# Kernel tuning notes

Measured on AMD Instinct MI355X. Metric: run time of the kernel, lower is better.

## Reference

```python
import jax, jax.numpy as jnp
import numpy as np

B, S, H, NH = 2, 2048, 1024, 16
HD = H // NH  # 64


def rope_cos_sin(seq_len, dim, base=10000.0, dtype=jnp.float32):
    inv_freq = 1.0 / (base ** (jnp.arange(0, dim, 2, dtype=jnp.float32) / dim))
    t = jnp.arange(seq_len, dtype=jnp.float32)
    freqs = jnp.outer(t, inv_freq)              # [S, dim/2]
    emb = jnp.concatenate([freqs, freqs], -1)   # [S, dim]
    # broadcast shape [1, S, 1, dim]
    return jnp.cos(emb)[None, :, None, :].astype(dtype), jnp.sin(emb)[None, :, None, :].astype(dtype)


def rotate_half(x):
    x1, x2 = x[..., : x.shape[-1] // 2], x[..., x.shape[-1] // 2:]
    return jnp.concatenate([-x2, x1], axis=-1)


def setup_inputs() -> dict:
    key = jax.random.key(0)
    ks = jax.random.split(key, 5)
    sc = 1.0 / np.sqrt(H)
    x = jax.random.normal(ks[0], (B, S, H), jnp.float32)
    Wq = jax.random.normal(ks[1], (H, H), jnp.float32) * sc
    Wk = jax.random.normal(ks[2], (H, H), jnp.float32) * sc
    Wv = jax.random.normal(ks[3], (H, H), jnp.float32) * sc
    Wo = jax.random.normal(ks[4], (H, H), jnp.float32) * sc
    z = jnp.zeros((H,), jnp.float32)
    mask = jnp.tril(jnp.ones((S, S), bool))[None, None]  # causal [1,1,S,S]
    return {"x": x, "Wq": Wq, "bq": z, "Wk": Wk, "bk": z, "Wv": Wv, "bv": z,
            "Wo": Wo, "bo": z, "mask": mask}


def reference(x, Wq, bq, Wk, bk, Wv, bv, Wo, bo, mask):
    b, s, _ = x.shape
    q = (x @ Wq.T + bq).reshape(b, s, NH, HD)
    k = (x @ Wk.T + bk).reshape(b, s, NH, HD)
    v = (x @ Wv.T + bv).reshape(b, s, NH, HD)
    cos, sin = rope_cos_sin(s, HD, dtype=x.dtype)
    q = q * cos + rotate_half(q) * sin
    k = k * cos + rotate_half(k) * sin
    # [b, h, s, s] scores, explicit as in original
    scores = jnp.einsum("bqhd,bkhd->bhqk", q, k) / jnp.sqrt(jnp.asarray(HD, x.dtype))
    scores = jnp.where(mask, scores, jnp.asarray(-jnp.inf, x.dtype))
    attn = jax.nn.softmax(scores, axis=-1)
    out = jnp.einsum("bhqk,bkhd->bqhd", attn, v).reshape(b, s, H)
    return out @ Wo.T + bo
```

## Files before the change

kernel.cpp:

```cpp
#include <hip/hip_runtime.h>

typedef __bf16 bf16;
typedef __bf16 bf16x4 __attribute__((ext_vector_type(4)));
typedef __bf16 bf16x8 __attribute__((ext_vector_type(8)));
typedef float floatx4 __attribute__((ext_vector_type(4)));

#define MFMA16(a, b, c) __builtin_amdgcn_mfma_f32_16x16x32_bf16(a, b, c, 0, 0, 0)

__device__ __forceinline__ void load_lds16(const void* g, void* l) {
    __builtin_amdgcn_global_load_lds(
        (const __attribute__((address_space(1))) unsigned int*)g,
        (__attribute__((address_space(3))) unsigned int*)l, 16, 0, 0);
}

__device__ __forceinline__ bf16x8 scale8(bf16x8 a, float s) {
    bf16x8 o;
    #pragma unroll
    for (int i = 0; i < 8; i++) o[i] = (bf16)((float)a[i] * s);
    return o;
}

__global__ __launch_bounds__(256) void cvt_all_kernel(
    const float* __restrict__ x, const float* __restrict__ wq,
    const float* __restrict__ wk, const float* __restrict__ wv,
    const float* __restrict__ wo,
    bf16* __restrict__ xb, bf16* __restrict__ wqb, bf16* __restrict__ wkb,
    bf16* __restrict__ wvb, bf16* __restrict__ wob)
{
    int bid = blockIdx.x;
    const float* src; bf16* dst; int off;
    if (bid < 4096)      { src = x;  dst = xb;  off = bid; }
    else if (bid < 5120) { src = wq; dst = wqb; off = bid - 4096; }
    else if (bid < 6144) { src = wk; dst = wkb; off = bid - 5120; }
    else if (bid < 7168) { src = wv; dst = wvb; off = bid - 6144; }
    else                 { src = wo; dst = wob; off = bid - 7168; }
    int idx = (off * 256 + threadIdx.x) * 4;
    float4 v = *(const float4*)&src[idx];
    bf16x4 o;
    o[0] = (bf16)v.x; o[1] = (bf16)v.y; o[2] = (bf16)v.z; o[3] = (bf16)v.w;
    *(bf16x4*)&dst[idx] = o;
}

__global__ __launch_bounds__(256) void cvt_kernel(const float* __restrict__ x,
                                                  bf16* __restrict__ xb) {
    int idx = (blockIdx.x * 256 + threadIdx.x) * 4;
    float4 v = *(const float4*)&x[idx];
    bf16x4 o;
    o[0] = (bf16)v.x; o[1] = (bf16)v.y; o[2] = (bf16)v.z; o[3] = (bf16)v.w;
    *(bf16x4*)&xb[idx] = o;
}


#define STAGE_TILES(Asrc, Bsrc, arow, brow)                                   \
    _Pragma("unroll")                                                         \
    for (int t = 0; t < 4; t++) {                                             \
        int R0 = w * 32 + t * 8;                                              \
        int row = R0 + (lane >> 3);                                           \
        int gc = (lane & 7) ^ (row & 7);                                      \
        load_lds16(&Asrc[(size_t)(arow + row) * 1024 + k0 + gc * 8], &As[R0][0]); \
        load_lds16(&Bsrc[(size_t)(brow + row) * 1024 + k0 + gc * 8], &Bs[R0][0]); \
    }

__global__ __launch_bounds__(256) void gemm_qkv_fast(
    const bf16* __restrict__ xb,
    const bf16* __restrict__ Wq, const bf16* __restrict__ Wk,
    const bf16* __restrict__ Wv,
    const float* __restrict__ bq, const float* __restrict__ bk,
    const float* __restrict__ bv,
    bf16* __restrict__ q_ws, bf16* __restrict__ k_ws, bf16* __restrict__ vt_ws)
{
    int m0 = blockIdx.x * 128;
    int n0 = blockIdx.y * 128;
    int sec = n0 >> 10;
    int nw0 = n0 & 1023;
    const bf16* W     = (sec == 0) ? Wq : (sec == 1) ? Wk : Wv;
    const float* bias = (sec == 0) ? bq : (sec == 1) ? bk : bv;

    __shared__ bf16 As[128][64];
    __shared__ bf16 Bs[128][64];

    int tid = threadIdx.x;
    int lane = tid & 63, w = tid >> 6;
    int l15 = lane & 15, quad = lane >> 4;
    int wm = (w >> 1) * 64, wn = (w & 1) * 64;

    floatx4 acc[4][4];
    #pragma unroll
    for (int i = 0; i < 4; i++)
        #pragma unroll
        for (int j = 0; j < 4; j++) acc[i][j] = (floatx4){0.f, 0.f, 0.f, 0.f};

    for (int k0 = 0; k0 < 1024; k0 += 64) {
        __syncthreads();
        STAGE_TILES(xb, W, m0, nw0)
        __syncthreads();
        #pragma unroll
        for (int kk = 0; kk < 2; kk++) {
            int cb = kk * 4 + quad;
            bf16x8 af[4], bfr[4];
            #pragma unroll
            for (int mt = 0; mt < 4; mt++) {
                int row = wm + mt * 16 + l15;
                af[mt] = *(const bf16x8*)&As[row][(cb ^ (row & 7)) * 8];
            }
            #pragma unroll
            for (int nt = 0; nt < 4; nt++) {
                int row = wn + nt * 16 + l15;
                bfr[nt] = *(const bf16x8*)&Bs[row][(cb ^ (row & 7)) * 8];
            }
            #pragma unroll
            for (int mt = 0; mt < 4; mt++)
                #pragma unroll
                for (int nt = 0; nt < 4; nt++)
                    acc[mt][nt] = MFMA16(af[mt], bfr[nt], acc[mt][nt]);
        }
    }

    if (sec < 2) {
        bf16* outp = (sec == 0) ? q_ws : k_ws;
        float inv[2];
        inv[0] = __expf(-(float)l15 * (9.210340371976184f / 32.0f));
        inv[1] = __expf(-(float)(16 + l15) * (9.210340371976184f / 32.0f));
        #pragma unroll
        for (int mt = 0; mt < 4; mt++) {
            #pragma unroll
            for (int r = 0; r < 4; r++) {
                int m = m0 + wm + mt * 16 + quad * 4 + r;
                int bb = m >> 11, s = m & 2047;
                #pragma unroll
                for (int nt = 0; nt < 2; nt++) {
                    int nl1 = nw0 + wn + nt * 16 + l15;
                    int nl2 = nl1 + 32;
                    float x1 = acc[mt][nt][r] + bias[nl1];
                    float x2 = acc[mt][nt + 2][r] + bias[nl2];
                    float ang = (float)s * inv[nt];
                    float sn, cs;
                    __sincosf(ang, &sn, &cs);
                    int hh = nl1 >> 6, d = nl1 & 63;
                    size_t base = ((size_t)(bb * 16 + hh) * 2048 + s) * 64;
                    outp[base + d]      = (bf16)(x1 * cs - x2 * sn);
                    outp[base + d + 32] = (bf16)(x2 * cs + x1 * sn);
                }
            }
        }
    } else {
        #pragma unroll
        for (int mt = 0; mt < 4; mt++) {
            int mbase = m0 + wm + mt * 16 + quad * 4;
            int bb = mbase >> 11, s0 = mbase & 2047;
            #pragma unroll
            for (int nt = 0; nt < 4; nt++) {
                int nl = nw0 + wn + nt * 16 + l15;
                int hh = nl >> 6, d = nl & 63;
                bf16x4 pk;
                #pragma unroll
                for (int r = 0; r < 4; r++) pk[r] = (bf16)(acc[mt][nt][r] + bias[nl]);
                *(bf16x4*)&vt_ws[((size_t)(bb * 16 + hh) * 64 + d) * 2048 + s0] = pk;
            }
        }
    }
}

__global__ __launch_bounds__(256) void gemm_out_fast(
    const bf16* __restrict__ A, const bf16* __restrict__ W,
    const float* __restrict__ bias, float* __restrict__ out)
{
    int m0 = blockIdx.x * 128;
    int n0 = blockIdx.y * 128;

    __shared__ bf16 As[128][64];
    __shared__ bf16 Bs[128][64];

    int tid = threadIdx.x;
    int lane = tid & 63, w = tid >> 6;
    int l15 = lane & 15, quad = lane >> 4;
    int wm = (w >> 1) * 64, wn = (w & 1) * 64;

    floatx4 acc[4][4];
    #pragma unroll
    for (int i = 0; i < 4; i++)
        #pragma unroll
        for (int j = 0; j < 4; j++) acc[i][j] = (floatx4){0.f, 0.f, 0.f, 0.f};

    for (int k0 = 0; k0 < 1024; k0 += 64) {
        __syncthreads();
        STAGE_TILES(A, W, m0, n0)
        __syncthreads();
        #pragma unroll
        for (int kk = 0; kk < 2; kk++) {
            int cb = kk * 4 + quad;
            bf16x8 af[4], bfr[4];
            #pragma unroll
            for (int mt = 0; mt < 4; mt++) {
                int row = wm + mt * 16 + l15;
                af[mt] = *(const bf16x8*)&As[row][(cb ^ (row & 7)) * 8];
            }
            #pragma unroll
            for (int nt = 0; nt < 4; nt++) {
                int row = wn + nt * 16 + l15;
                bfr[nt] = *(const bf16x8*)&Bs[row][(cb ^ (row & 7)) * 8];
            }
            #pragma unroll
            for (int mt = 0; mt < 4; mt++)
                #pragma unroll
                for (int nt = 0; nt < 4; nt++)
                    acc[mt][nt] = MFMA16(af[mt], bfr[nt], acc[mt][nt]);
        }
    }

    #pragma unroll
    for (int mt = 0; mt < 4; mt++) {
        #pragma unroll
        for (int r = 0; r < 4; r++) {
            int m = m0 + wm + mt * 16 + quad * 4 + r;
            #pragma unroll
            for (int nt = 0; nt < 4; nt++) {
                int nl = n0 + wn + nt * 16 + l15;
                out[(size_t)m * 1024 + nl] = acc[mt][nt][r] + bias[nl];
            }
        }
    }
}

__global__ __launch_bounds__(256) void gemm_qkv_f32w(
    const bf16* __restrict__ xb,
    const float* __restrict__ Wq, const float* __restrict__ Wk,
    const float* __restrict__ Wv,
    const float* __restrict__ bq, const float* __restrict__ bk,
    const float* __restrict__ bv,
    bf16* __restrict__ q_ws, bf16* __restrict__ k_ws, bf16* __restrict__ vt_ws)
{
    int m0 = blockIdx.x * 128;
    int n0 = blockIdx.y * 128;
    int sec = n0 >> 10;
    int nw0 = n0 & 1023;
    const float* W    = (sec == 0) ? Wq : (sec == 1) ? Wk : Wv;
    const float* bias = (sec == 0) ? bq : (sec == 1) ? bk : bv;

    __shared__ bf16 As[128][72];
    __shared__ bf16 Bs[128][72];

    int tid = threadIdx.x;
    int lane = tid & 63, w = tid >> 6;
    int l15 = lane & 15, quad = lane >> 4;
    int wm = (w >> 1) * 64, wn = (w & 1) * 64;
    int sr = tid >> 1;
    int sk = (tid & 1) * 32;

    floatx4 acc[4][4];
    #pragma unroll
    for (int i = 0; i < 4; i++)
        #pragma unroll
        for (int j = 0; j < 4; j++) acc[i][j] = (floatx4){0.f, 0.f, 0.f, 0.f};

    for (int k0 = 0; k0 < 1024; k0 += 64) {
        __syncthreads();
        const bf16* ap = &xb[(size_t)(m0 + sr) * 1024 + k0 + sk];
        bf16x8 a0 = *(const bf16x8*)(ap);
        bf16x8 a1 = *(const bf16x8*)(ap + 8);
        bf16x8 a2 = *(const bf16x8*)(ap + 16);
        bf16x8 a3 = *(const bf16x8*)(ap + 24);
        const float* wp = &W[(size_t)(nw0 + sr) * 1024 + k0 + sk];
        bf16x8 bv_[4];
        #pragma unroll
        for (int c = 0; c < 4; c++) {
            float4 f0 = *(const float4*)(wp + c * 8);
            float4 f1 = *(const float4*)(wp + c * 8 + 4);
            bf16x8 t;
            t[0] = (bf16)f0.x; t[1] = (bf16)f0.y; t[2] = (bf16)f0.z; t[3] = (bf16)f0.w;
            t[4] = (bf16)f1.x; t[5] = (bf16)f1.y; t[6] = (bf16)f1.z; t[7] = (bf16)f1.w;
            bv_[c] = t;
        }
        *(bf16x8*)&As[sr][sk + 0]  = a0;
        *(bf16x8*)&As[sr][sk + 8]  = a1;
        *(bf16x8*)&As[sr][sk + 16] = a2;
        *(bf16x8*)&As[sr][sk + 24] = a3;
        #pragma unroll
        for (int c = 0; c < 4; c++) *(bf16x8*)&Bs[sr][sk + c * 8] = bv_[c];
        __syncthreads();
        #pragma unroll
        for (int kk = 0; kk < 64; kk += 32) {
            bf16x8 af[4], bfr[4];
            #pragma unroll
            for (int mt = 0; mt < 4; mt++)
                af[mt] = *(const bf16x8*)&As[wm + mt * 16 + l15][kk + quad * 8];
            #pragma unroll
            for (int nt = 0; nt < 4; nt++)
                bfr[nt] = *(const bf16x8*)&Bs[wn + nt * 16 + l15][kk + quad * 8];
            #pragma unroll
            for (int mt = 0; mt < 4; mt++)
                #pragma unroll
                for (int nt = 0; nt < 4; nt++)
                    acc[mt][nt] = MFMA16(af[mt], bfr[nt], acc[mt][nt]);
        }
    }

    if (sec < 2) {
        bf16* outp = (sec == 0) ? q_ws : k_ws;
        float inv[2];
        inv[0] = __expf(-(float)l15 * (9.210340371976184f / 32.0f));
        inv[1] = __expf(-(float)(16 + l15) * (9.210340371976184f / 32.0f));
        #pragma unroll
        for (int mt = 0; mt < 4; mt++) {
            #pragma unroll
            for (int r = 0; r < 4; r++) {
                int m = m0 + wm + mt * 16 + quad * 4 + r;
                int bb = m >> 11, s = m & 2047;
                #pragma unroll
                for (int nt = 0; nt < 2; nt++) {
                    int nl1 = nw0 + wn + nt * 16 + l15;
                    int nl2 = nl1 + 32;
                    float x1 = acc[mt][nt][r] + bias[nl1];
                    float x2 = acc[mt][nt + 2][r] + bias[nl2];
                    float ang = (float)s * inv[nt];
                    float sn, cs;
                    __sincosf(ang, &sn, &cs);
                    int hh = nl1 >> 6, d = nl1 & 63;
                    size_t base = ((size_t)(bb * 16 + hh) * 2048 + s) * 64;
                    outp[base + d]      = (bf16)(x1 * cs - x2 * sn);
                    outp[base + d + 32] = (bf16)(x2 * cs + x1 * sn);
                }
            }
        }
    } else {
        #pragma unroll
        for (int mt = 0; mt < 4; mt++) {
            int mbase = m0 + wm + mt * 16 + quad * 4;
            int bb = mbase >> 11, s0 = mbase & 2047;
            #pragma unroll
            for (int nt = 0; nt < 4; nt++) {
                int nl = nw0 + wn + nt * 16 + l15;
                int hh = nl >> 6, d = nl & 63;
                bf16x4 pk;
                #pragma unroll
                for (int r = 0; r < 4; r++) pk[r] = (bf16)(acc[mt][nt][r] + bias[nl]);
                *(bf16x4*)&vt_ws[((size_t)(bb * 16 + hh) * 64 + d) * 2048 + s0] = pk;
            }
        }
    }
}

__global__ __launch_bounds__(256) void gemm_out_f32w(
    const bf16* __restrict__ A, const float* __restrict__ W,
    const float* __restrict__ bias, float* __restrict__ out)
{
    int m0 = blockIdx.x * 128;
    int n0 = blockIdx.y * 128;

    __shared__ bf16 As[128][72];
    __shared__ bf16 Bs[128][72];

    int tid = threadIdx.x;
    int lane = tid & 63, w = tid >> 6;
    int l15 = lane & 15, quad = lane >> 4;
    int wm = (w >> 1) * 64, wn = (w & 1) * 64;
    int sr = tid >> 1;
    int sk = (tid & 1) * 32;

    floatx4 acc[4][4];
    #pragma unroll
    for (int i = 0; i < 4; i++)
        #pragma unroll
        for (int j = 0; j < 4; j++) acc[i][j] = (floatx4){0.f, 0.f, 0.f, 0.f};

    for (int k0 = 0; k0 < 1024; k0 += 64) {
        __syncthreads();
        const bf16* ap = &A[(size_t)(m0 + sr) * 1024 + k0 + sk];
        bf16x8 a0 = *(const bf16x8*)(ap);
        bf16x8 a1 = *(const bf16x8*)(ap + 8);
        bf16x8 a2 = *(const bf16x8*)(ap + 16);
        bf16x8 a3 = *(const bf16x8*)(ap + 24);
        const float* wp = &W[(size_t)(n0 + sr) * 1024 + k0 + sk];
        bf16x8 bv_[4];
        #pragma unroll
        for (int c = 0; c < 4; c++) {
            float4 f0 = *(const float4*)(wp + c * 8);
            float4 f1 = *(const float4*)(wp + c * 8 + 4);
            bf16x8 t;
            t[0] = (bf16)f0.x; t[1] = (bf16)f0.y; t[2] = (bf16)f0.z; t[3] = (bf16)f0.w;
            t[4] = (bf16)f1.x; t[5] = (bf16)f1.y; t[6] = (bf16)f1.z; t[7] = (bf16)f1.w;
            bv_[c] = t;
        }
        *(bf16x8*)&As[sr][sk + 0]  = a0;
        *(bf16x8*)&As[sr][sk + 8]  = a1;
        *(bf16x8*)&As[sr][sk + 16] = a2;
        *(bf16x8*)&As[sr][sk + 24] = a3;
        #pragma unroll
        for (int c = 0; c < 4; c++) *(bf16x8*)&Bs[sr][sk + c * 8] = bv_[c];
        __syncthreads();
        #pragma unroll
        for (int kk = 0; kk < 64; kk += 32) {
            bf16x8 af[4], bfr[4];
            #pragma unroll
            for (int mt = 0; mt < 4; mt++)
                af[mt] = *(const bf16x8*)&As[wm + mt * 16 + l15][kk + quad * 8];
            #pragma unroll
            for (int nt = 0; nt < 4; nt++)
                bfr[nt] = *(const bf16x8*)&Bs[wn + nt * 16 + l15][kk + quad * 8];
            #pragma unroll
            for (int mt = 0; mt < 4; mt++)
                #pragma unroll
                for (int nt = 0; nt < 4; nt++)
                    acc[mt][nt] = MFMA16(af[mt], bfr[nt], acc[mt][nt]);
        }
    }

    #pragma unroll
    for (int mt = 0; mt < 4; mt++) {
        #pragma unroll
        for (int r = 0; r < 4; r++) {
            int m = m0 + wm + mt * 16 + quad * 4 + r;
            #pragma unroll
            for (int nt = 0; nt < 4; nt++) {
                int nl = n0 + wn + nt * 16 + l15;
                out[(size_t)m * 1024 + nl] = acc[mt][nt][r] + bias[nl];
            }
        }
    }
}

__global__ __launch_bounds__(256) void attn_kernel(
    const bf16* __restrict__ q_ws, const bf16* __restrict__ k_ws,
    const bf16* __restrict__ vt_ws, bf16* __restrict__ o_ws)
{
    __shared__ bf16 Ks[64][64];
    __shared__ bf16 Vt[64][64];
    __shared__ bf16 Ps[4][16][72];

    int tid = threadIdx.x;
    int w = tid >> 6, lane = tid & 63;
    int l15 = lane & 15, quad = lane >> 4;
    int h = blockIdx.y, bb = blockIdx.z;
    int x = blockIdx.x;
    int qt = ((h < 8) == (bb == 0)) ? x : 31 - x;
    int bh = bb * 16 + h;
    const bf16* qp = q_ws + (size_t)bh * 2048 * 64;
    const bf16* kp = k_ws + (size_t)bh * 2048 * 64;
    const bf16* vp = vt_ws + (size_t)bh * 64 * 2048;
    int qrow = qt * 64 + w * 16;

    const float SCL = 0.125f * 1.4426950408889634f;
    bf16x8 qf0 = scale8(*(const bf16x8*)&qp[(size_t)(qrow + l15) * 64 + quad * 8], SCL);
    bf16x8 qf1 = scale8(*(const bf16x8*)&qp[(size_t)(qrow + l15) * 64 + 32 + quad * 8], SCL);

    const float MFIX = 20.0f;
    float l_lane = 0.f;
    floatx4 acc[4];
    #pragma unroll
    for (int nt = 0; nt < 4; nt++) acc[nt] = (floatx4){0.f, 0.f, 0.f, 0.f};

    int g0 = (w * 2) * 64 + lane;
    int g1 = (w * 2 + 1) * 64 + lane;
    int r0 = g0 >> 3, c0 = (g0 & 7) ^ (r0 & 7);
    int r1 = g1 >> 3, c1 = (g1 & 7) ^ (r1 & 7);
    bf16* ksBase0 = &Ks[0][0] + (w * 2) * 512;
    bf16* ksBase1 = &Ks[0][0] + (w * 2 + 1) * 512;
    bf16* vtBase0 = &Vt[0][0] + (w * 2) * 512;
    bf16* vtBase1 = &Vt[0][0] + (w * 2 + 1) * 512;

    for (int kt = 0; kt <= qt; kt++) {
        int kt0 = kt * 64;
        __syncthreads();
        load_lds16(&kp[(size_t)(kt0 + r0) * 64 + c0 * 8], ksBase0);
        load_lds16(&kp[(size_t)(kt0 + r1) * 64 + c1 * 8], ksBase1);
        load_lds16(&vp[(size_t)r0 * 2048 + kt0 + c0 * 8], vtBase0);
        load_lds16(&vp[(size_t)r1 * 2048 + kt0 + c1 * 8], vtBase1);
        __syncthreads();

        floatx4 st[4];
        #pragma unroll
        for (int kb = 0; kb < 4; kb++) {
            int row = kb * 16 + l15;
            int rx = row & 7;
            bf16x8 a0 = *(const bf16x8*)&Ks[row][(quad ^ rx) * 8];
            bf16x8 a1 = *(const bf16x8*)&Ks[row][((quad + 4) ^ rx) * 8];
            floatx4 z = {0.f, 0.f, 0.f, 0.f};
            z = MFMA16(a0, qf0, z);
            z = MFMA16(a1, qf1, z);
            st[kb] = z;
        }
        if (kt0 + 63 > qrow) {
            int q = qrow + l15;
            #pragma unroll
            for (int kb = 0; kb < 4; kb++)
                #pragma unroll
                for (int r = 0; r < 4; r++) {
                    int key = kt0 + kb * 16 + quad * 4 + r;
                    if (key > q) st[kb][r] = -1e30f;
                }
        }

        #pragma unroll
        for (int kb = 0; kb < 4; kb++) {
            bf16x4 pk;
            #pragma unroll
            for (int r = 0; r < 4; r++) {
                float pv = exp2f(st[kb][r] - MFIX);
                l_lane += pv;
                pk[r] = (bf16)pv;
            }
            *(bf16x4*)&Ps[w][l15][kb * 16 + quad * 4] = pk;
        }

        bf16x8 pb0 = *(const bf16x8*)&Ps[w][l15][quad * 8];
        bf16x8 pb1 = *(const bf16x8*)&Ps[w][l15][32 + quad * 8];
        #pragma unroll
        for (int nt = 0; nt < 4; nt++) {
            int row = nt * 16 + l15;
            int rx = row & 7;
            bf16x8 v0 = *(const bf16x8*)&Vt[row][(quad ^ rx) * 8];
            bf16x8 v1 = *(const bf16x8*)&Vt[row][((quad + 4) ^ rx) * 8];
            acc[nt] = MFMA16(v0, pb0, acc[nt]);
            acc[nt] = MFMA16(v1, pb1, acc[nt]);
        }
    }

    l_lane += __shfl_xor(l_lane, 16, 64);
    l_lane += __shfl_xor(l_lane, 32, 64);
    float inv = 1.f / l_lane;
    int s = qrow + l15;
    #pragma unroll
    for (int nt = 0; nt < 4; nt++) {
        bf16x4 pk;
        #pragma unroll
        for (int r = 0; r < 4; r++) pk[r] = (bf16)(acc[nt][r] * inv);
        *(bf16x4*)&o_ws[((size_t)(bb * 2048 + s)) * 1024 + h * 64 + nt * 16 + quad * 4] = pk;
    }
}

extern "C" void kernel_launch(void* const* d_in, const int* in_sizes, int n_in,
                              void* d_out, int out_size, void* d_ws, size_t ws_size,
                              hipStream_t stream) {
    const float* x  = (const float*)d_in[0];
    const float* Wq = (const float*)d_in[1];
    const float* bq = (const float*)d_in[2];
    const float* Wk = (const float*)d_in[3];
    const float* bk = (const float*)d_in[4];
    const float* Wv = (const float*)d_in[5];
    const float* bv = (const float*)d_in[6];
    const float* Wo = (const float*)d_in[7];
    const float* bo = (const float*)d_in[8];
    float* out = (float*)d_out;

    const size_t NELEM = (size_t)2 * 2048 * 1024;
    const size_t WELEM = (size_t)1024 * 1024;
    bf16* xb    = (bf16*)d_ws;
    bf16* q_ws  = xb + NELEM;
    bf16* k_ws  = q_ws + NELEM;
    bf16* vt_ws = k_ws + NELEM;
    bf16* o_ws  = xb;
    bf16* wqb   = vt_ws + NELEM;
    bf16* wkb   = wqb + WELEM;
    bf16* wvb   = wkb + WELEM;
    bf16* wob   = wvb + WELEM;

    bool fast = ws_size >= (size_t)40 * 1024 * 1024;

    if (fast) {
        cvt_all_kernel<<<8192, 256, 0, stream>>>(x, Wq, Wk, Wv, Wo,
                                                 xb, wqb, wkb, wvb, wob);
        gemm_qkv_fast<<<dim3(32, 24), 256, 0, stream>>>(
            xb, wqb, wkb, wvb, bq, bk, bv, q_ws, k_ws, vt_ws);
        attn_kernel<<<dim3(32, 16, 2), 256, 0, stream>>>(q_ws, k_ws, vt_ws, o_ws);
        gemm_out_fast<<<dim3(32, 8), 256, 0, stream>>>(o_ws, wob, bo, out);
    } else {
        cvt_kernel<<<4096, 256, 0, stream>>>(x, xb);
        gemm_qkv_f32w<<<dim3(32, 24), 256, 0, stream>>>(
            xb, Wq, Wk, Wv, bq, bk, bv, q_ws, k_ws, vt_ws);
        attn_kernel<<<dim3(32, 16, 2), 256, 0, stream>>>(q_ws, k_ws, vt_ws, o_ws);
        gemm_out_f32w<<<dim3(32, 8), 256, 0, stream>>>(o_ws, Wo, bo, out);
    }
}
```

Measured before the change: 215.0 us.

## Double-buffer K/V tiles and pair causal query tiles per attention block

The attention kernel now double-buffers K and V tiles in LDS, so the global-to-LDS load of the next key tile is issued before the current tile is computed. That removes one barrier per iteration. Each block now handles two query tiles (x and 31-x), which balances causal work per block, and the grid is halved to 16 in x. The trade-off is more LDS per block and fewer blocks in flight (512), which may reduce occupancy and latency hiding.

```diff
diff --git a/kernel.cpp b/kernel.cpp
--- a/kernel.cpp
+++ b/kernel.cpp
@@ -423,8 +423,8 @@
     const bf16* __restrict__ q_ws, const bf16* __restrict__ k_ws,
     const bf16* __restrict__ vt_ws, bf16* __restrict__ o_ws)
 {
-    __shared__ bf16 Ks[64][64];
-    __shared__ bf16 Vt[64][64];
+    __shared__ bf16 Ks[2][64][64];
+    __shared__ bf16 Vt[2][64][64];
     __shared__ bf16 Ps[4][16][72];
 
     int tid = threadIdx.x;
@@ -432,99 +432,119 @@
     int l15 = lane & 15, quad = lane >> 4;
     int h = blockIdx.y, bb = blockIdx.z;
     int x = blockIdx.x;
-    int qt = ((h < 8) == (bb == 0)) ? x : 31 - x;
     int bh = bb * 16 + h;
     const bf16* qp = q_ws + (size_t)bh * 2048 * 64;
     const bf16* kp = k_ws + (size_t)bh * 2048 * 64;
     const bf16* vp = vt_ws + (size_t)bh * 64 * 2048;
-    int qrow = qt * 64 + w * 16;
-
-    const float SCL = 0.125f * 1.4426950408889634f;
-    bf16x8 qf0 = scale8(*(const bf16x8*)&qp[(size_t)(qrow + l15) * 64 + quad * 8], SCL);
-    bf16x8 qf1 = scale8(*(const bf16x8*)&qp[(size_t)(qrow + l15) * 64 + 32 + quad * 8], SCL);
-
-    const float MFIX = 20.0f;
-    float l_lane = 0.f;
-    floatx4 acc[4];
-    #pragma unroll
-    for (int nt = 0; nt < 4; nt++) acc[nt] = (floatx4){0.f, 0.f, 0.f, 0.f};
 
     int g0 = (w * 2) * 64 + lane;
     int g1 = (w * 2 + 1) * 64 + lane;
     int r0 = g0 >> 3, c0 = (g0 & 7) ^ (r0 & 7);
     int r1 = g1 >> 3, c1 = (g1 & 7) ^ (r1 & 7);
-    bf16* ksBase0 = &Ks[0][0] + (w * 2) * 512;
-    bf16* ksBase1 = &Ks[0][0] + (w * 2 + 1) * 512;
-    bf16* vtBase0 = &Vt[0][0] + (w * 2) * 512;
-    bf16* vtBase1 = &Vt[0][0] + (w * 2 + 1) * 512;
-
-    for (int kt = 0; kt <= qt; kt++) {
-        int kt0 = kt * 64;
-        __syncthreads();
-        load_lds16(&kp[(size_t)(kt0 + r0) * 64 + c0 * 8], ksBase0);
-        load_lds16(&kp[(size_t)(kt0 + r1) * 64 + c1 * 8], ksBase1);
-        load_lds16(&vp[(size_t)r0 * 2048 + kt0 + c0 * 8], vtBase0);
-        load_lds16(&vp[(size_t)r1 * 2048 + kt0 + c1 * 8], vtBase1);
-        __syncthreads();
-
-        floatx4 st[4];
-        #pragma unroll
-        for (int kb = 0; kb < 4; kb++) {
-            int row = kb * 16 + l15;
-            int rx = row & 7;
-            bf16x8 a0 = *(const bf16x8*)&Ks[row][(quad ^ rx) * 8];
-            bf16x8 a1 = *(const bf16x8*)&Ks[row][((quad + 4) ^ rx) * 8];
-            floatx4 z = {0.f, 0.f, 0.f, 0.f};
-            z = MFMA16(a0, qf0, z);
-            z = MFMA16(a1, qf1, z);
-            st[kb] = z;
-        }
-        if (kt0 + 63 > qrow) {
-            int q = qrow + l15;
-            #pragma unroll
-            for (int kb = 0; kb < 4; kb++)
+    int o0 = (w * 2) * 512;
+    int o1 = (w * 2 + 1) * 512;
+
+    const float SCL = 0.125f * 1.4426950408889634f;
+    const float MFIX = 20.0f;
+
+    #pragma unroll 1
+    for (int pass = 0; pass < 2; ++pass) {
+        int qt = pass ? (31 - x) : x;
+        int qrow = qt * 64 + w * 16;
+
+        bf16x8 qf0 = scale8(*(const bf16x8*)&qp[(size_t)(qrow + l15) * 64 + quad * 8], SCL);
+        bf16x8 qf1 = scale8(*(const bf16x8*)&qp[(size_t)(qrow + l15) * 64 + 32 + quad * 8], SCL);
+
+        float l_lane = 0.f;
+        floatx4 acc[4];
+        #pragma unroll
+        for (int nt = 0; nt < 4; nt++) acc[nt] = (floatx4){0.f, 0.f, 0.f, 0.f};
+
+        __syncthreads();
+        {
+            bf16* kb = &Ks[0][0][0];
+            bf16* vb = &Vt[0][0][0];
+            load_lds16(&kp[(size_t)r0 * 64 + c0 * 8], kb + o0);
+            load_lds16(&kp[(size_t)r1 * 64 + c1 * 8], kb + o1);
+            load_lds16(&vp[(size_t)r0 * 2048 + c0 * 8], vb + o0);
+            load_lds16(&vp[(size_t)r1 * 2048 + c1 * 8], vb + o1);
+        }
+
+        for (int kt = 0; kt <= qt; kt++) {
+            int buf = kt & 1;
+            __syncthreads();
+
+            if (kt < qt) {
+                int kn0 = (kt + 1) * 64;
+                bf16* kb = &Ks[buf ^ 1][0][0];
+                bf16* vb = &Vt[buf ^ 1][0][0];
+                load_lds16(&kp[(size_t)(kn0 + r0) * 64 + c0 * 8], kb + o0);
+                load_lds16(&kp[(size_t)(kn0 + r1) * 64 + c1 * 8], kb + o1);
+                load_lds16(&vp[(size_t)r0 * 2048 + kn0 + c0 * 8], vb + o0);
+                load_lds16(&vp[(size_t)r1 * 2048 + kn0 + c1 * 8], vb + o1);
+            }
+
+            int kt0 = kt * 64;
+
+            floatx4 st[4];
+            #pragma unroll
+            for (int kb = 0; kb < 4; kb++) {
+                int row = kb * 16 + l15;
+                int rx = row & 7;
+                bf16x8 a0 = *(const bf16x8*)&Ks[buf][row][(quad ^ rx) * 8];
+                bf16x8 a1 = *(const bf16x8*)&Ks[buf][row][((quad + 4) ^ rx) * 8];
+                floatx4 z = {0.f, 0.f, 0.f, 0.f};
+                z = MFMA16(a0, qf0, z);
+                z = MFMA16(a1, qf1, z);
+                st[kb] = z;
+            }
+            if (kt0 + 63 > qrow) {
+                int q = qrow + l15;
+                #pragma unroll
+                for (int kb = 0; kb < 4; kb++)
+                    #pragma unroll
+                    for (int r = 0; r < 4; r++) {
+                        int key = kt0 + kb * 16 + quad * 4 + r;
+                        if (key > q) st[kb][r] = -1e30f;
+                    }
+            }
+
+            #pragma unroll
+            for (int kb = 0; kb < 4; kb++) {
+                bf16x4 pk;
                 #pragma unroll
                 for (int r = 0; r < 4; r++) {
-                    int key = kt0 + kb * 16 + quad * 4 + r;
-                    if (key > q) st[kb][r] = -1e30f;
+                    float pv = exp2f(st[kb][r] - MFIX);
+                    l_lane += pv;
+                    pk[r] = (bf16)pv;
                 }
-        }
-
-        #pragma unroll
-        for (int kb = 0; kb < 4; kb++) {
+                *(bf16x4*)&Ps[w][l15][kb * 16 + quad * 4] = pk;
+            }
+
+            bf16x8 pb0 = *(const bf16x8*)&Ps[w][l15][quad * 8];
+            bf16x8 pb1 = *(const bf16x8*)&Ps[w][l15][32 + quad * 8];
+            #pragma unroll
+            for (int nt = 0; nt < 4; nt++) {
+                int row = nt * 16 + l15;
+                int rx = row & 7;
+                bf16x8 v0 = *(const bf16x8*)&Vt[buf][row][(quad ^ rx) * 8];
+                bf16x8 v1 = *(const bf16x8*)&Vt[buf][row][((quad + 4) ^ rx) * 8];
+                acc[nt] = MFMA16(v0, pb0, acc[nt]);
+                acc[nt] = MFMA16(v1, pb1, acc[nt]);
+            }
+        }
+
+        l_lane += __shfl_xor(l_lane, 16, 64);
+        l_lane += __shfl_xor(l_lane, 32, 64);
+        float inv = 1.f / l_lane;
+        int s = qrow + l15;
+        #pragma unroll
+        for (int nt = 0; nt < 4; nt++) {
             bf16x4 pk;
             #pragma unroll
-            for (int r = 0; r < 4; r++) {
-                float pv = exp2f(st[kb][r] - MFIX);
-                l_lane += pv;
-                pk[r] = (bf16)pv;
-            }
-            *(bf16x4*)&Ps[w][l15][kb * 16 + quad * 4] = pk;
-        }
-
-        bf16x8 pb0 = *(const bf16x8*)&Ps[w][l15][quad * 8];
-        bf16x8 pb1 = *(const bf16x8*)&Ps[w][l15][32 + quad * 8];
-        #pragma unroll
-        for (int nt = 0; nt < 4; nt++) {
-            int row = nt * 16 + l15;
-            int rx = row & 7;
-            bf16x8 v0 = *(const bf16x8*)&Vt[row][(quad ^ rx) * 8];
-            bf16x8 v1 = *(const bf16x8*)&Vt[row][((quad + 4) ^ rx) * 8];
-            acc[nt] = MFMA16(v0, pb0, acc[nt]);
-            acc[nt] = MFMA16(v1, pb1, acc[nt]);
-        }
-    }
-
-    l_lane += __shfl_xor(l_lane, 16, 64);
-    l_lane += __shfl_xor(l_lane, 32, 64);
-    float inv = 1.f / l_lane;
-    int s = qrow + l15;
-    #pragma unroll
-    for (int nt = 0; nt < 4; nt++) {
-        bf16x4 pk;
-        #pragma unroll
-        for (int r = 0; r < 4; r++) pk[r] = (bf16)(acc[nt][r] * inv);
-        *(bf16x4*)&o_ws[((size_t)(bb * 2048 + s)) * 1024 + h * 64 + nt * 16 + quad * 4] = pk;
+            for (int r = 0; r < 4; r++) pk[r] = (bf16)(acc[nt][r] * inv);
+            *(bf16x4*)&o_ws[((size_t)(bb * 2048 + s)) * 1024 + h * 64 + nt * 16 + quad * 4] = pk;
+        }
     }
 }
 
@@ -561,13 +581,13 @@
                                                  xb, wqb, wkb, wvb, wob);
         gemm_qkv_fast<<<dim3(32, 24), 256, 0, stream>>>(
             xb, wqb, wkb, wvb, bq, bk, bv, q_ws, k_ws, vt_ws);
-        attn_kernel<<<dim3(32, 16, 2), 256, 0, stream>>>(q_ws, k_ws, vt_ws, o_ws);
+        attn_kernel<<<dim3(16, 16, 2), 256, 0, stream>>>(q_ws, k_ws, vt_ws, o_ws);
         gemm_out_fast<<<dim3(32, 8), 256, 0, stream>>>(o_ws, wob, bo, out);
     } else {
         cvt_kernel<<<4096, 256, 0, stream>>>(x, xb);
         gemm_qkv_f32w<<<dim3(32, 24), 256, 0, stream>>>(
             xb, Wq, Wk, Wv, bq, bk, bv, q_ws, k_ws, vt_ws);
-        attn_kernel<<<dim3(32, 16, 2), 256, 0, stream>>>(q_ws, k_ws, vt_ws, o_ws);
+        attn_kernel<<<dim3(16, 16, 2), 256, 0, stream>>>(q_ws, k_ws, vt_ws, o_ws);
         gemm_out_f32w<<<dim3(32, 8), 256, 0, stream>>>(o_ws, Wo, bo, out);
     }
 }
```

Result: no change. 214.3 us (-0.3%).
